# Kernel optimization log

Measured on AMD Instinct MI355X. Metric: run time of the kernel, lower is better.

## Reference

```python
import jax, jax.numpy as jnp
import numpy as np

D_MODEL = 1024
NUM_HEADS = 16
HEAD_DIM = D_MODEL // NUM_HEADS
B, T = 2, 2048


def setup_inputs() -> dict:
    key = jax.random.key(0)
    kx, kq, kk, kv, ko = jax.random.split(key, 5)
    s = 1.0 / np.sqrt(D_MODEL)
    x = jax.random.normal(kx, (B, T, D_MODEL), dtype=jnp.float32)
    Wq = jax.random.normal(kq, (D_MODEL, D_MODEL), dtype=jnp.float32) * s
    Wk = jax.random.normal(kk, (D_MODEL, D_MODEL), dtype=jnp.float32) * s
    Wv = jax.random.normal(kv, (D_MODEL, D_MODEL), dtype=jnp.float32) * s
    Wo = jax.random.normal(ko, (D_MODEL, D_MODEL), dtype=jnp.float32) * s
    # causal boolean mask [T,T], True = keep (every row keeps >=1 key)
    attn_mask = jnp.tril(jnp.ones((T, T), dtype=bool))
    return {"x": x, "Wq": Wq, "Wk": Wk, "Wv": Wv, "Wo": Wo, "attn_mask": attn_mask}


def reference(x, Wq, Wk, Wv, Wo, attn_mask):
    Bb, Tt, Dd = x.shape
    h, dh = NUM_HEADS, HEAD_DIM
    # Linear(bias=False): y = x @ W.T
    q = (x @ Wq.T).reshape(Bb, Tt, h, dh).transpose(0, 2, 1, 3)  # [B,h,T,dh]
    k = (x @ Wk.T).reshape(Bb, Tt, h, dh).transpose(0, 2, 1, 3)
    v = (x @ Wv.T).reshape(Bb, Tt, h, dh).transpose(0, 2, 1, 3)
    scores = jnp.einsum('bhqd,bhkd->bhqk', q, k) / jnp.sqrt(jnp.float32(dh))
    keep = attn_mask[None, None, :, :]  # [1,1,T,T], True = keep
    scores = jnp.where(keep, scores, -jnp.inf)
    # original subtracts row max then softmax; jax.nn.softmax is equivalent (stable)
    attn = jax.nn.softmax(scores, axis=-1)
    out = jnp.einsum('bhqk,bhkd->bhqd', attn, v)  # [B,h,T,dh]
    out = out.transpose(0, 2, 1, 3).reshape(Bb, Tt, Dd)
    return out @ Wo.T
```

## Files before the change

kernel.cpp:

```cpp
#include <hip/hip_runtime.h>
#include <hip/hip_bf16.h>
#include <stdint.h>

typedef __bf16 bf16_t;
typedef bf16_t bf16x8 __attribute__((ext_vector_type(8)));
typedef float  f32x4  __attribute__((ext_vector_type(4)));
typedef float  f32x16 __attribute__((ext_vector_type(16)));

#define MFMA16(a, b, c) __builtin_amdgcn_mfma_f32_16x16x32_bf16((a), (b), (c), 0, 0, 0)
#define MFMA32(a, b, c) __builtin_amdgcn_mfma_f32_32x32x16_bf16((a), (b), (c), 0, 0, 0)

static __device__ __forceinline__ unsigned short f2bf(float f) {
    __hip_bfloat16 h = __float2bfloat16(f);
    return __builtin_bit_cast(unsigned short, h);
}
static __device__ __forceinline__ unsigned int pk2(float a, float b) {
    return ((unsigned int)f2bf(b) << 16) | (unsigned int)f2bf(a);
}

static __device__ __forceinline__ void gld_lds16(const void* g, void* l) {
    __builtin_amdgcn_global_load_lds(
        (const __attribute__((address_space(1))) uint32_t*)g,
        (__attribute__((address_space(3))) uint32_t*)l, 16, 0, 0);
}

#define TT     2048
#define DM     1024
#define NH     16
#define HD     64

__global__ __launch_bounds__(256) void cast_x(const float* __restrict__ src,
                                              unsigned short* __restrict__ dst, int n4) {
    int i = blockIdx.x * 256 + threadIdx.x;
    if (i >= n4) return;
    float4 v = reinterpret_cast<const float4*>(src)[i];
    ushort4 o;
    o.x = f2bf(v.x); o.y = f2bf(v.y); o.z = f2bf(v.z); o.w = f2bf(v.w);
    reinterpret_cast<ushort4*>(dst)[i] = o;
}

__global__ __launch_bounds__(256) void cast_w(const float* __restrict__ wq,
                                              const float* __restrict__ wk,
                                              const float* __restrict__ wv,
                                              const float* __restrict__ wo_in,
                                              unsigned short* __restrict__ wqkv,
                                              unsigned short* __restrict__ wo_out) {
    const int y = blockIdx.y;
    const float* src = (y == 0) ? wq : (y == 1) ? wk : (y == 2) ? wv : wo_in;
    unsigned short* dst = (y < 3) ? (wqkv + (size_t)y * (1u << 20)) : wo_out;
    int i = blockIdx.x * 256 + threadIdx.x;
    float4 v = reinterpret_cast<const float4*>(src)[i];
    ushort4 o;
    o.x = f2bf(v.x); o.y = f2bf(v.y); o.z = f2bf(v.z); o.w = f2bf(v.w);
    reinterpret_cast<ushort4*>(dst)[i] = o;
}

template <int BM, int BN, int WM, int WN, int MODE>
__global__ __launch_bounds__(WM * WN * 64, 1)
void gemm2ph(const unsigned short* __restrict__ A, const unsigned short* __restrict__ W,
             float* __restrict__ out, int Nn,
             unsigned short* __restrict__ qp, unsigned short* __restrict__ kp,
             unsigned short* __restrict__ vp, int gridM) {
    constexpr int THREADS = WM * WN * 64;
    constexpr int MF = BM / WM / 16;
    constexpr int NF = BN / WN / 16;
    constexpr int ABYTES = BM * 128;
    constexpr int BUFB = ABYTES + BN * 128;
    extern __shared__ char lds[];

    const int tid = threadIdx.x;
    const int l = tid & 63, w = tid >> 6;
    const int r = l & 15, g = l >> 4, rb = r & 7;
    const int wm = w / WN, wn = w % WN;

    const int bid = blockIdx.x;
    const int cpx = gridDim.x >> 3;
    const int swz = (bid & 7) * cpx + (bid >> 3);
    const int m0 = (swz % gridM) * BM;
    const int n0 = (swz / gridM) * BN;

    const int lrow = l >> 3;
    const int gch = (l & 7) ^ lrow;
    const unsigned short* aG = A + (size_t)(m0 + w * 8 + lrow) * 1024 + gch * 8;
    const unsigned short* bG = W + (size_t)(n0 + w * 8 + lrow) * 1024 + gch * 8;
    const int lOff = (w * 64 + l) * 16;

#define STAGE(buf, t)                                                              \
    do {                                                                           \
        char* ab_ = lds + (buf) * BUFB;                                            \
        char* bb_ = ab_ + ABYTES;                                                  \
        _Pragma("unroll")                                                          \
        for (int q_ = 0; q_ < BM * 8 / THREADS; ++q_)                              \
            gld_lds16(aG + (size_t)q_ * (THREADS / 8) * 1024 + (t) * 64,           \
                      ab_ + q_ * THREADS * 16 + lOff);                             \
        _Pragma("unroll")                                                          \
        for (int q_ = 0; q_ < BN * 8 / THREADS; ++q_)                              \
            gld_lds16(bG + (size_t)q_ * (THREADS / 8) * 1024 + (t) * 64,           \
                      bb_ + q_ * THREADS * 16 + lOff);                             \
    } while (0)

    f32x4 acc[MF][NF];
#pragma unroll
    for (int i = 0; i < MF; i++)
#pragma unroll
        for (int j = 0; j < NF; j++) acc[i][j] = (f32x4){0.f, 0.f, 0.f, 0.f};

    STAGE(0, 0);
    __syncthreads();

    int cur = 0;
    for (int t = 0; t < 16; ++t) {
        if (t + 1 < 16) STAGE(cur ^ 1, t + 1);
        const char* aRd = lds + cur * BUFB + (wm * (BM / WM) + r) * 128;
        const char* bRd = lds + cur * BUFB + ABYTES + (wn * (BN / WN) + r) * 128;
#pragma unroll
        for (int kk = 0; kk < 2; ++kk) {
            const int ch = ((kk * 4 + g) ^ rb) * 16;
            bf16x8 af[MF], bfr[NF];
#pragma unroll
            for (int i = 0; i < MF; ++i)
                af[i] = *reinterpret_cast<const bf16x8*>(aRd + i * 2048 + ch);
#pragma unroll
            for (int j = 0; j < NF; ++j)
                bfr[j] = *reinterpret_cast<const bf16x8*>(bRd + j * 2048 + ch);
            __builtin_amdgcn_s_setprio(1);
#pragma unroll
            for (int i = 0; i < MF; ++i)
#pragma unroll
                for (int j = 0; j < NF; ++j) acc[i][j] = MFMA16(af[i], bfr[j], acc[i][j]);
            __builtin_amdgcn_s_setprio(0);
        }
        __syncthreads();
        cur ^= 1;
    }
#undef STAGE

#pragma unroll
    for (int i = 0; i < MF; ++i) {
#pragma unroll
        for (int j = 0; j < NF; ++j) {
#pragma unroll
            for (int reg = 0; reg < 4; ++reg) {
                const int mg = m0 + wm * (BM / WM) + i * 16 + g * 4 + reg;
                const int ng = n0 + wn * (BN / WN) + j * 16 + r;
                const float v = acc[i][j][reg];
                if constexpr (MODE == 1) {
                    out[(size_t)mg * Nn + ng] = v;
                } else {
                    const int sel = ng >> 10;
                    const int c10 = ng & 1023;
                    const int h = c10 >> 6, d = c10 & 63;
                    const int bb_ = mg >> 11, tq = mg & 2047;
                    const int bh = bb_ * NH + h;
                    if (sel == 0)      qp[(bh * TT + tq) * HD + d] = f2bf(v * 0.125f);
                    else if (sel == 1) kp[(bh * TT + tq) * HD + d] = f2bf(v);
                    else               vp[(bh * HD + d) * TT + tq] = f2bf(v);
                }
            }
        }
    }
}

__global__ __launch_bounds__(256) void attn_kernel(const unsigned short* __restrict__ q,
                                                   const unsigned short* __restrict__ k,
                                                   const unsigned short* __restrict__ v,
                                                   unsigned short* __restrict__ o) {
    __shared__ unsigned short lK[64 * 64];
    __shared__ unsigned short lV[64 * 64];

    const int tid = threadIdx.x;
    const int l   = tid & 63;
    const int w   = tid >> 6;
    const int c   = l & 31;
    const int hi  = l >> 5;

    const int id   = blockIdx.x;
    const int half = id >> 8;
    const int sub  = id & 255;
    const int bh   = sub >> 3;
    const int j8   = sub & 7;
    const int qt   = half ? (15 - j8) : j8;
    const int q0w  = qt * 128 + w * 32;
    const int nkt  = 2 * qt + 2;

    const unsigned short* qbase = q + (size_t)bh * TT * HD;
    const unsigned short* kbase = k + (size_t)bh * TT * HD;
    const unsigned short* vbase = v + (size_t)bh * HD * TT;

    bf16x8 qf[4];
#pragma unroll
    for (int ks = 0; ks < 4; ++ks)
        qf[ks] = *reinterpret_cast<const bf16x8*>(qbase + (q0w + c) * HD + ks * 16 + hi * 8);

    f32x16 Oacc[2];
#pragma unroll
    for (int jd = 0; jd < 2; ++jd)
#pragma unroll
        for (int e = 0; e < 16; ++e) Oacc[jd][e] = 0.f;
    float m_r = -1e30f, l_r = 0.f;

    const int cA = tid, cB = tid + 256;
    const int rA = cA >> 3, colA = (cA & 7) * 8;
    const int rB = cB >> 3, colB = (cB & 7) * 8;
    const int dstA = rA * 128 + ((colA * 2) ^ ((rA & 7) << 4));
    const int dstB = rB * 128 + ((colB * 2) ^ ((rB & 7) << 4));

    uint4 ka, kb, va, vb;
    ka = *reinterpret_cast<const uint4*>(kbase + rA * HD + colA);
    kb = *reinterpret_cast<const uint4*>(kbase + rB * HD + colB);
    va = *reinterpret_cast<const uint4*>(vbase + rA * TT + colA);
    vb = *reinterpret_cast<const uint4*>(vbase + rB * TT + colB);

    for (int kt = 0; kt < nkt; ++kt) {
        const int k0 = kt * 64;
        __syncthreads();
        *reinterpret_cast<uint4*>((char*)lK + dstA) = ka;
        *reinterpret_cast<uint4*>((char*)lK + dstB) = kb;
        *reinterpret_cast<uint4*>((char*)lV + dstA) = va;
        *reinterpret_cast<uint4*>((char*)lV + dstB) = vb;
        __syncthreads();
        if (kt + 1 < nkt) {
            const int kn = k0 + 64;
            ka = *reinterpret_cast<const uint4*>(kbase + (kn + rA) * HD + colA);
            kb = *reinterpret_cast<const uint4*>(kbase + (kn + rB) * HD + colB);
            va = *reinterpret_cast<const uint4*>(vbase + rA * TT + kn + colA);
            vb = *reinterpret_cast<const uint4*>(vbase + rB * TT + kn + colB);
        }
        if (k0 > q0w + 31) continue;

        f32x16 s[2];
#pragma unroll
        for (int j = 0; j < 2; ++j) {
#pragma unroll
            for (int e = 0; e < 16; ++e) s[j][e] = 0.f;
#pragma unroll
            for (int ks = 0; ks < 4; ++ks) {
                const int row = j * 32 + c;
                bf16x8 kf = *reinterpret_cast<const bf16x8*>(
                    (char*)lK + row * 128 + (((ks * 16 + hi * 8) * 2) ^ ((row & 7) << 4)));
                s[j] = MFMA32(kf, qf[ks], s[j]);
            }
        }

        if (k0 + 63 > q0w) {
            const int qg = q0w + c;
#pragma unroll
            for (int j = 0; j < 2; ++j)
#pragma unroll
                for (int e = 0; e < 16; ++e) {
                    const int kv = k0 + j * 32 + (e & 3) + 8 * (e >> 2) + 4 * hi;
                    if (kv > qg) s[j][e] = -1e30f;
                }
        }

        float mx = s[0][0];
#pragma unroll
        for (int e = 1; e < 16; ++e) mx = fmaxf(mx, s[0][e]);
#pragma unroll
        for (int e = 0; e < 16; ++e) mx = fmaxf(mx, s[1][e]);
        mx = fmaxf(mx, __shfl_xor(mx, 32));
        const float mnew = fmaxf(m_r, mx);
        const float corr = __expf(m_r - mnew);
        float sum = 0.f;
#pragma unroll
        for (int j = 0; j < 2; ++j)
#pragma unroll
            for (int e = 0; e < 16; ++e) {
                const float p = __expf(s[j][e] - mnew);
                s[j][e] = p;
                sum += p;
            }
        sum += __shfl_xor(sum, 32);
        l_r = l_r * corr + sum;
        m_r = mnew;
#pragma unroll
        for (int jd = 0; jd < 2; ++jd)
#pragma unroll
            for (int e = 0; e < 16; ++e) Oacc[jd][e] *= corr;

        bf16x8 pa[4];
#pragma unroll
        for (int ks = 0; ks < 4; ++ks) {
            const int j = ks >> 1;
            const int base = (ks & 1) * 8;
            const unsigned int pA0 = pk2(s[j][base + 0], s[j][base + 1]);
            const unsigned int pA1 = pk2(s[j][base + 2], s[j][base + 3]);
            const unsigned int pB0 = pk2(s[j][base + 4], s[j][base + 5]);
            const unsigned int pB1 = pk2(s[j][base + 6], s[j][base + 7]);
            const unsigned int m0_ = hi ? pB0 : pA0;
            const unsigned int m1_ = hi ? pB1 : pA1;
            const unsigned int o0 = hi ? pA0 : pB0;
            const unsigned int o1 = hi ? pA1 : pB1;
            const unsigned int r0 = __shfl_xor(o0, 32);
            const unsigned int r1 = __shfl_xor(o1, 32);
            uint4 u;
            u.x = hi ? r0 : m0_;
            u.y = hi ? r1 : m1_;
            u.z = hi ? m0_ : r0;
            u.w = hi ? m1_ : r1;
            pa[ks] = __builtin_bit_cast(bf16x8, u);
        }

#pragma unroll
        for (int jd = 0; jd < 2; ++jd) {
#pragma unroll
            for (int ks = 0; ks < 4; ++ks) {
                const int row = jd * 32 + c;
                bf16x8 vf = *reinterpret_cast<const bf16x8*>(
                    (char*)lV + row * 128 + (((ks * 16 + hi * 8) * 2) ^ ((row & 7) << 4)));
                Oacc[jd] = MFMA32(vf, pa[ks], Oacc[jd]);
            }
        }
    }

    const int b_ = bh >> 4, h_ = bh & 15;
    const float inv = 1.f / l_r;
    const int qg = q0w + c;
    unsigned short* orow = o + ((size_t)b_ * TT + qg) * DM + h_ * HD;
#pragma unroll
    for (int jd = 0; jd < 2; ++jd)
#pragma unroll
        for (int ep = 0; ep < 8; ++ep) {
            const int e0 = ep * 2;
            const int d0 = jd * 32 + (e0 & 3) + 8 * (e0 >> 2) + 4 * hi;
            const unsigned int pkv = pk2(Oacc[jd][e0] * inv, Oacc[jd][e0 + 1] * inv);
            *reinterpret_cast<unsigned int*>(orow + d0) = pkv;
        }
}

extern "C" void kernel_launch(void* const* d_in, const int* in_sizes, int n_in,
                              void* d_out, int out_size, void* d_ws, size_t ws_size,
                              hipStream_t stream) {
    const float* x  = (const float*)d_in[0];
    const float* Wq = (const float*)d_in[1];
    const float* Wk = (const float*)d_in[2];
    const float* Wv = (const float*)d_in[3];
    const float* Wo = (const float*)d_in[4];

    char* ws = (char*)d_ws;
    unsigned short* xb   = (unsigned short*)(ws);
    unsigned short* wqkv = (unsigned short*)(ws + (8u  << 20));
    unsigned short* wo   = (unsigned short*)(ws + (14u << 20));
    unsigned short* qb   = (unsigned short*)(ws + (16u << 20));
    unsigned short* kb   = (unsigned short*)(ws + (24u << 20));
    unsigned short* vb   = (unsigned short*)(ws + (32u << 20));
    unsigned short* ab   = (unsigned short*)(ws + (40u << 20));
    float* outp = (float*)d_out;

    cast_x<<<4096, 256, 0, stream>>>(x, xb, 1048576);
    cast_w<<<dim3(1024, 4), 256, 0, stream>>>(Wq, Wk, Wv, Wo, wqkv, wo);

    gemm2ph<256, 256, 2, 4, 0><<<192, 512, 131072, stream>>>(
        xb, wqkv, nullptr, 3072, qb, kb, vb, 16);
    attn_kernel<<<512, 256, 0, stream>>>(qb, kb, vb, ab);
    gemm2ph<128, 128, 2, 2, 1><<<256, 256, 65536, stream>>>(
        ab, wo, outp, 1024, nullptr, nullptr, nullptr, 32);
}
```

Before: 220.7 us.

## Rewrite GEMM main loop as 4-stage async LDS pipeline with K=32 steps

Replaces the double-buffered K=64 GEMM loop with a four-buffer ring of K=32 slices. Loads run three stages ahead, and explicit vmcnt waits plus a raw s_barrier replace the full __syncthreads per step. The LDS swizzle is changed to match 64-byte rows. The output-projection GEMM now uses 512 threads (4x2 waves) instead of 256. The aim is to hide global-to-LDS latency behind MFMA work, at the cost of twice as many barriers and hand-tuned waitcnt values that must match the number of issued loads.

```diff
diff --git a/kernel.cpp b/kernel.cpp
--- a/kernel.cpp
+++ b/kernel.cpp
@@ -56,21 +56,25 @@
 }
 
 template <int BM, int BN, int WM, int WN, int MODE>
-__global__ __launch_bounds__(WM * WN * 64, 1)
-void gemm2ph(const unsigned short* __restrict__ A, const unsigned short* __restrict__ W,
-             float* __restrict__ out, int Nn,
-             unsigned short* __restrict__ qp, unsigned short* __restrict__ kp,
-             unsigned short* __restrict__ vp, int gridM) {
+__global__ __launch_bounds__(512, 1)
+void gemm4d(const unsigned short* __restrict__ A, const unsigned short* __restrict__ W,
+            float* __restrict__ out, int Nn,
+            unsigned short* __restrict__ qp, unsigned short* __restrict__ kp,
+            unsigned short* __restrict__ vp, int gridM) {
     constexpr int THREADS = WM * WN * 64;
+    static_assert(THREADS == 512, "template assumes 512 threads");
     constexpr int MF = BM / WM / 16;
     constexpr int NF = BN / WN / 16;
-    constexpr int ABYTES = BM * 128;
-    constexpr int BUFB = ABYTES + BN * 128;
+    constexpr int ABYTES = BM * 64;
+    constexpr int BUFB = ABYTES + BN * 64;
+    constexpr int APT = BM / 128;
+    constexpr int BPT = BN / 128;
+    constexpr int IPT = APT + BPT;
     extern __shared__ char lds[];
 
     const int tid = threadIdx.x;
     const int l = tid & 63, w = tid >> 6;
-    const int r = l & 15, g = l >> 4, rb = r & 7;
+    const int r = l & 15, g = l >> 4;
     const int wm = w / WN, wn = w % WN;
 
     const int bid = blockIdx.x;
@@ -79,24 +83,23 @@
     const int m0 = (swz % gridM) * BM;
     const int n0 = (swz / gridM) * BN;
 
-    const int lrow = l >> 3;
-    const int gch = (l & 7) ^ lrow;
-    const unsigned short* aG = A + (size_t)(m0 + w * 8 + lrow) * 1024 + gch * 8;
-    const unsigned short* bG = W + (size_t)(n0 + w * 8 + lrow) * 1024 + gch * 8;
-    const int lOff = (w * 64 + l) * 16;
-
-#define STAGE(buf, t)                                                              \
-    do {                                                                           \
-        char* ab_ = lds + (buf) * BUFB;                                            \
-        char* bb_ = ab_ + ABYTES;                                                  \
-        _Pragma("unroll")                                                          \
-        for (int q_ = 0; q_ < BM * 8 / THREADS; ++q_)                              \
-            gld_lds16(aG + (size_t)q_ * (THREADS / 8) * 1024 + (t) * 64,           \
-                      ab_ + q_ * THREADS * 16 + lOff);                             \
-        _Pragma("unroll")                                                          \
-        for (int q_ = 0; q_ < BN * 8 / THREADS; ++q_)                              \
-            gld_lds16(bG + (size_t)q_ * (THREADS / 8) * 1024 + (t) * 64,           \
-                      bb_ + q_ * THREADS * 16 + lOff);                             \
+    const int srow = tid >> 2;
+    const int gcol = (tid & 3) ^ (srow & 3);
+    const unsigned short* aG = A + (size_t)(m0 + srow) * 1024 + gcol * 8;
+    const unsigned short* bG = W + (size_t)(n0 + srow) * 1024 + gcol * 8;
+
+#define STAGE4(buf, t)                                                         \
+    do {                                                                       \
+        char* ab_ = lds + (buf) * BUFB;                                        \
+        char* bb_ = ab_ + ABYTES;                                              \
+        _Pragma("unroll")                                                      \
+        for (int q_ = 0; q_ < APT; ++q_)                                       \
+            gld_lds16(aG + (size_t)q_ * 128 * 1024 + (t) * 32,                 \
+                      ab_ + q_ * 8192 + tid * 16);                             \
+        _Pragma("unroll")                                                      \
+        for (int q_ = 0; q_ < BPT; ++q_)                                       \
+            gld_lds16(bG + (size_t)q_ * 128 * 1024 + (t) * 32,                 \
+                      bb_ + q_ * 8192 + tid * 16);                             \
     } while (0)
 
     f32x4 acc[MF][NF];
@@ -105,35 +108,48 @@
 #pragma unroll
         for (int j = 0; j < NF; j++) acc[i][j] = (f32x4){0.f, 0.f, 0.f, 0.f};
 
-    STAGE(0, 0);
-    __syncthreads();
-
-    int cur = 0;
-    for (int t = 0; t < 16; ++t) {
-        if (t + 1 < 16) STAGE(cur ^ 1, t + 1);
-        const char* aRd = lds + cur * BUFB + (wm * (BM / WM) + r) * 128;
-        const char* bRd = lds + cur * BUFB + ABYTES + (wn * (BN / WN) + r) * 128;
-#pragma unroll
-        for (int kk = 0; kk < 2; ++kk) {
-            const int ch = ((kk * 4 + g) ^ rb) * 16;
-            bf16x8 af[MF], bfr[NF];
-#pragma unroll
-            for (int i = 0; i < MF; ++i)
-                af[i] = *reinterpret_cast<const bf16x8*>(aRd + i * 2048 + ch);
-#pragma unroll
-            for (int j = 0; j < NF; ++j)
-                bfr[j] = *reinterpret_cast<const bf16x8*>(bRd + j * 2048 + ch);
-            __builtin_amdgcn_s_setprio(1);
-#pragma unroll
-            for (int i = 0; i < MF; ++i)
-#pragma unroll
-                for (int j = 0; j < NF; ++j) acc[i][j] = MFMA16(af[i], bfr[j], acc[i][j]);
-            __builtin_amdgcn_s_setprio(0);
-        }
-        __syncthreads();
-        cur ^= 1;
+    STAGE4(0, 0);
+    STAGE4(1, 1);
+    STAGE4(2, 2);
+
+    const int rdsw = ((g ^ (r & 3)) << 4);
+
+    for (int t = 0; t < 32; ++t) {
+        if constexpr (IPT == 4) {
+            if (t <= 29)      asm volatile("s_waitcnt vmcnt(8)" ::: "memory");
+            else if (t == 30) asm volatile("s_waitcnt vmcnt(4)" ::: "memory");
+            else              asm volatile("s_waitcnt vmcnt(0)" ::: "memory");
+        } else {
+            if (t <= 29)      asm volatile("s_waitcnt vmcnt(4)" ::: "memory");
+            else if (t == 30) asm volatile("s_waitcnt vmcnt(2)" ::: "memory");
+            else              asm volatile("s_waitcnt vmcnt(0)" ::: "memory");
+        }
+        __builtin_amdgcn_sched_barrier(0);
+        __builtin_amdgcn_s_barrier();
+        __builtin_amdgcn_sched_barrier(0);
+
+        const char* ab_ = lds + (t & 3) * BUFB;
+        const char* bb_ = ab_ + ABYTES;
+        bf16x8 af[MF], bfr[NF];
+#pragma unroll
+        for (int i = 0; i < MF; ++i)
+            af[i] = *reinterpret_cast<const bf16x8*>(
+                ab_ + (wm * (BM / WM) + i * 16 + r) * 64 + rdsw);
+#pragma unroll
+        for (int j = 0; j < NF; ++j)
+            bfr[j] = *reinterpret_cast<const bf16x8*>(
+                bb_ + (wn * (BN / WN) + j * 16 + r) * 64 + rdsw);
+
+        if (t < 29) STAGE4((t + 3) & 3, t + 3);
+
+        __builtin_amdgcn_s_setprio(1);
+#pragma unroll
+        for (int i = 0; i < MF; ++i)
+#pragma unroll
+            for (int j = 0; j < NF; ++j) acc[i][j] = MFMA16(af[i], bfr[j], acc[i][j]);
+        __builtin_amdgcn_s_setprio(0);
     }
-#undef STAGE
+#undef STAGE4
 
 #pragma unroll
     for (int i = 0; i < MF; ++i) {
@@ -150,8 +166,8 @@
                     const int sel = ng >> 10;
                     const int c10 = ng & 1023;
                     const int h = c10 >> 6, d = c10 & 63;
-                    const int bb_ = mg >> 11, tq = mg & 2047;
-                    const int bh = bb_ * NH + h;
+                    const int bb2 = mg >> 11, tq = mg & 2047;
+                    const int bh = bb2 * NH + h;
                     if (sel == 0)      qp[(bh * TT + tq) * HD + d] = f2bf(v * 0.125f);
                     else if (sel == 1) kp[(bh * TT + tq) * HD + d] = f2bf(v);
                     else               vp[(bh * HD + d) * TT + tq] = f2bf(v);
@@ -350,9 +366,9 @@
     cast_x<<<4096, 256, 0, stream>>>(x, xb, 1048576);
     cast_w<<<dim3(1024, 4), 256, 0, stream>>>(Wq, Wk, Wv, Wo, wqkv, wo);
 
-    gemm2ph<256, 256, 2, 4, 0><<<192, 512, 131072, stream>>>(
+    gemm4d<256, 256, 2, 4, 0><<<192, 512, 131072, stream>>>(
         xb, wqkv, nullptr, 3072, qb, kb, vb, 16);
     attn_kernel<<<512, 256, 0, stream>>>(qb, kb, vb, ab);
-    gemm2ph<128, 128, 2, 2, 1><<<256, 256, 65536, stream>>>(
+    gemm4d<128, 128, 4, 2, 1><<<256, 512, 65536, stream>>>(
         ab, wo, outp, 1024, nullptr, nullptr, nullptr, 32);
 }
```

Measured after the change: 219.9 us. Within noise of the previous version (-0.4%).
